# Kernel optimization log

Hardware: AMD Instinct MI355X
Metric: run time of the kernel (lower is better)

## Reference

```python
import jax, jax.numpy as jnp
import numpy as np

MARGIN = 0.1
LAMBDA_EFFECT = 0.5

B, T_V, K, T_S = 32, 8192, 64, 128


def setup_inputs() -> dict:
    key = jax.random.key(0)
    k1, k2, k3, k4, k5 = jax.random.split(key, 5)
    pred_orig = jax.random.normal(k1, (B, T_V), dtype=jnp.float32)
    pred_intervened = jax.random.normal(k2, (K, B, T_V), dtype=jnp.float32)
    intervened_indices = jax.random.randint(k3, (K,), 0, T_S, dtype=jnp.int32)
    # GT alignment mask: sparse-ish binary alignment between frames and sentences
    gt_mask = jax.random.bernoulli(k4, 0.2, (B, T_V, T_S)).astype(jnp.int32)
    # prefix-valid video mask: valid length per batch in [T_V//2, T_V]
    lengths = jax.random.randint(k5, (B,), T_V // 2, T_V + 1, dtype=jnp.int32)
    mask_video = (jnp.arange(T_V, dtype=jnp.int32)[None, :] < lengths[:, None]).astype(jnp.int32)
    return {
        "pred_orig": pred_orig,
        "pred_intervened": pred_intervened,
        "intervened_indices": intervened_indices,
        "gt_mask": gt_mask,
        "mask_video": mask_video,
    }


def reference(pred_orig, pred_intervened, intervened_indices, gt_mask, mask_video):
    # pred_orig: [B,T], pred_intervened: [K,B,T], gt_mask: [B,T,S], mask_video: [B,T]
    prob_orig = jax.nn.sigmoid(pred_orig)                 # [B,T]
    prob_int = jax.nn.sigmoid(pred_intervened)            # [K,B,T]
    effect = jnp.abs(prob_orig[None, :, :] - prob_int)    # [K,B,T]

    valid = mask_video.astype(bool)                       # [B,T] (prefix mask == :T_v_valid slice)
    # gather intervened sentence columns: [B,T,K] -> [K,B,T]
    gt_sel = jnp.transpose(gt_mask[:, :, intervened_indices], (2, 0, 1))

    aligned = (gt_sel > 0) & valid[None]                  # [K,B,T]
    non_aligned = (gt_sel == 0) & valid[None]             # [K,B,T]

    cnt_a = aligned.sum(axis=-1)                          # [K,B]
    cnt_n = non_aligned.sum(axis=-1)                      # [K,B]

    ea = jnp.sum(effect * aligned, axis=-1) / jnp.maximum(cnt_a, 1)
    en = jnp.sum(effect * non_aligned, axis=-1) / jnp.maximum(cnt_n, 1)

    per_pair = jnp.where((cnt_a > 0) & (cnt_n > 0),
                         jax.nn.relu(MARGIN - (ea - en)),
                         jnp.zeros_like(ea))
    num_interventions = pred_orig.shape[0] * pred_intervened.shape[0]
    alignment_consistency = per_pair.sum() / max(num_interventions, 1)
    total_intervention_loss = alignment_consistency * LAMBDA_EFFECT
    return alignment_consistency, total_intervention_loss
```

## Files before the change

kernel.cpp:

```cpp
#include <hip/hip_runtime.h>
#include <cstdint>

#define BB 32
#define TV 8192
#define KK 64
#define TS 128
#define MARGIN_F 0.1f
#define LAMBDA_F 0.5f

#define TT 256
static constexpr int KSTR = BB * TV;
static constexpr int NTILE = TV / TT;

__global__ __launch_bounds__(512, 8) void fused_kernel(
    const float* __restrict__ po, const float* __restrict__ pi,
    const int* __restrict__ idx, const int* __restrict__ gt,
    const int* __restrict__ mv,
    float* __restrict__ gsa, float* __restrict__ gsv,
    float* __restrict__ gca, int* __restrict__ len) {
  const int tid = threadIdx.x;
  const int lane = tid & 63;
  const int w = tid >> 6;

  const int bid = blockIdx.x;
  const int b = bid >> 5;
  const int tile = ((bid & 31) + b) & 31;
  const int t0 = tile * TT;

  __shared__ unsigned ph[8][65];
  __shared__ unsigned sV[8];
  __shared__ float so[TT];
  __shared__ float saL[KK][65];
  __shared__ float svL[KK][65];

  const int grow = b * TV + t0 + 32 * w;
  const int mvv = (lane < 32) ? mv[grow + lane] : 0;
  const unsigned V32 = (unsigned)__ballot(mvv != 0);
  if (lane == 0) {
    sV[w] = V32;
    if (V32) atomicAdd(&len[b], __popc(V32));
  }
  if (tid < TT) so[tid] = __fdividef(1.f, 1.f + __expf(-po[b * TV + t0 + tid]));

  const int c = idx[lane];
  const int csel = c & 3, csh = c >> 2;
  unsigned plane = 0u;
  if (V32 != 0u) {
    const int4* rowp = (const int4*)(gt + (size_t)grow * TS);
#pragma unroll 4
    for (int ch = 0; ch < 16; ++ch) {
      const int4 v = rowp[ch * 64 + lane];
      const unsigned long long b0 = __ballot(v.x > 0);
      const unsigned long long b1 = __ballot(v.y > 0);
      const unsigned long long b2 = __ballot(v.z > 0);
      const unsigned long long b3 = __ballot(v.w > 0);
      const unsigned long long sel =
          (csel == 0) ? b0 : (csel == 1) ? b1 : (csel == 2) ? b2 : b3;
      plane |= (unsigned)((sel >> csh) & 1ull) << (2 * ch);
      plane |= (unsigned)((sel >> (32 + csh)) & 1ull) << (2 * ch + 1);
    }
    plane &= V32;
  }
  ph[w][lane] = plane;
  __syncthreads();

  if ((sV[0] | sV[1] | sV[2] | sV[3] | sV[4] | sV[5] | sV[6] | sV[7]) == 0u)
    return;

  const int g2 = lane >> 3;
  const int sh = (lane & 7) * 4;
  const unsigned vb4 = (sV[g2] >> sh) & 15u;
  const float4 so4 = *(const float4*)&so[lane * 4];
  const float* pib = pi + (size_t)b * TV + t0 + lane * 4;
  const int kbase = w * 8;

#pragma unroll 4
  for (int i = 0; i < 8; ++i) {
    const int k = kbase + i;
    const float4 x = *(const float4*)(pib + (size_t)k * KSTR);
    const unsigned ab4 = (ph[g2][k] >> sh) & 15u;
    const float e0 = fabsf(so4.x - __fdividef(1.f, 1.f + __expf(-x.x)));
    const float e1 = fabsf(so4.y - __fdividef(1.f, 1.f + __expf(-x.y)));
    const float e2 = fabsf(so4.z - __fdividef(1.f, 1.f + __expf(-x.z)));
    const float e3 = fabsf(so4.w - __fdividef(1.f, 1.f + __expf(-x.w)));
    float a = 0.f, vv = 0.f;
    if (ab4 & 1u) a += e0;
    if (vb4 & 1u) vv += e0;
    if (ab4 & 2u) a += e1;
    if (vb4 & 2u) vv += e1;
    if (ab4 & 4u) a += e2;
    if (vb4 & 4u) vv += e2;
    if (ab4 & 8u) a += e3;
    if (vb4 & 8u) vv += e3;
    saL[k][lane] = a;
    svL[k][lane] = vv;
  }
  __syncthreads();

  if (tid < KK) {
    const int k = tid;
    float S = 0.f;
    int ca = 0;
#pragma unroll 8
    for (int j = 0; j < 64; ++j) S += saL[k][j];
#pragma unroll
    for (int gg = 0; gg < 8; ++gg) ca += __popc(ph[gg][k]);
    atomicAdd(&gsa[k * BB + b], S);
    if (ca) atomicAdd(&gca[k * BB + b], (float)ca);
  } else if (tid < 2 * KK) {
    const int k = tid - KK;
    float S = 0.f;
#pragma unroll 8
    for (int j = 0; j < 64; ++j) S += svL[k][j];
    atomicAdd(&gsv[k * BB + b], S);
  }
}

__global__ __launch_bounds__(256) void fin_kernel(
    const float* __restrict__ gsa, const float* __restrict__ gsv,
    const float* __restrict__ gca, const int* __restrict__ len,
    float* __restrict__ out) {
  float s = 0.f;
  for (int i = threadIdx.x; i < KK * BB; i += 256) {
    const int b = i & (BB - 1);
    const float ca = gca[i];
    const float cn = (float)len[b] - ca;
    if (ca > 0.f && cn > 0.f) {
      const float sa = gsa[i];
      const float sv = gsv[i];
      const float d = MARGIN_F - (sa / ca - (sv - sa) / cn);
      s += d > 0.f ? d : 0.f;
    }
  }
#pragma unroll
  for (int off = 32; off > 0; off >>= 1) s += __shfl_down(s, off);
  __shared__ float ws4[4];
  if ((threadIdx.x & 63) == 0) ws4[threadIdx.x >> 6] = s;
  __syncthreads();
  if (threadIdx.x == 0) {
    const float S = ws4[0] + ws4[1] + ws4[2] + ws4[3];
    const float ac = S * (1.0f / (float)(KK * BB));
    out[0] = ac;
    out[1] = ac * LAMBDA_F;
  }
}

extern "C" void kernel_launch(void* const* d_in, const int* in_sizes, int n_in,
                              void* d_out, int out_size, void* d_ws, size_t ws_size,
                              hipStream_t stream) {
  const float* pred_orig = (const float*)d_in[0];
  const float* pred_int  = (const float*)d_in[1];
  const int*   idx       = (const int*)d_in[2];
  const int*   gt        = (const int*)d_in[3];
  const int*   mv        = (const int*)d_in[4];
  float* out = (float*)d_out;

  float* gsa = (float*)d_ws;
  float* gsv = gsa + KK * BB;
  float* gca = gsv + KK * BB;
  int*   len = (int*)(gca + KK * BB);

  hipMemsetAsync(d_ws, 0, (size_t)(3 * KK * BB) * sizeof(float) + BB * sizeof(int),
                 stream);
  fused_kernel<<<BB * NTILE, 512, 0, stream>>>(
      pred_orig, pred_int, idx, gt, mv, gsa, gsv, gca, len);
  fin_kernel<<<1, 256, 0, stream>>>(gsa, gsv, gca, len, out);
}
```

Before: 289.2 us.

## Split fused kernel into bitplane build and per-(k,b) reduction skipping invalid tail

Replaces the single fused kernel with two stages. The first builds per-(b,k) alignment bitplanes and validity bits from gt_mask into workspace, and records each batch's last valid word. The second runs one block per (k,b) pair and reads pred_intervened rows only up to the valid length, skipping chunks with no valid frames. Each block writes its partial sums directly instead of using atomics. This removes the wasted reads of invalid frames in pred_intervened, at the cost of an extra launch, a workspace round-trip for the planes, and recomputing sigmoid(pred_orig) once per k.

```diff
diff --git a/kernel.cpp b/kernel.cpp
--- a/kernel.cpp
+++ b/kernel.cpp
@@ -8,111 +8,131 @@
 #define MARGIN_F 0.1f
 #define LAMBDA_F 0.5f
 
-#define TT 256
-static constexpr int KSTR = BB * TV;
-static constexpr int NTILE = TV / TT;
+typedef unsigned long long u64;
+typedef unsigned int u32;
 
-__global__ __launch_bounds__(512, 8) void fused_kernel(
+static constexpr int KB_PAIRS = KK * BB;
+static constexpr int W32_PER_B = TV / 32;
+static constexpr int W64_PER_B = TV / 64;
+
+
+__global__ __launch_bounds__(128, 4) void plane_kernel(
+    const int* __restrict__ idx, const int* __restrict__ gt,
+    const int* __restrict__ mv, u32* __restrict__ vbit, u32* __restrict__ pl,
+    int* __restrict__ len, int* __restrict__ mw) {
+  const int lane = threadIdx.x & 63;
+  const int h = threadIdx.x >> 6;
+  const int blk = blockIdx.x;
+  const int b = blk >> 7;
+  const int g = blk & 127;
+  const int w32 = g * 2 + h;
+  const int grow = b * TV + g * 64 + h * 32;
+
+  const int mvv = (lane < 32) ? mv[grow + lane] : 0;
+  const u32 V = (u32)__ballot(mvv != 0);
+  if (lane == 0) {
+    vbit[b * W32_PER_B + w32] = V;
+    if (V) {
+      atomicAdd(&len[b], __popc(V));
+      atomicMax(&mw[b], w32);
+    }
+  }
+
+  u32 plane = 0;
+  if (V) {
+    const int c = idx[lane];
+    const int csel = c & 3, csh = c >> 2;
+    const int4* rowp = (const int4*)(gt + (size_t)grow * TS);
+#pragma unroll
+    for (int ch = 0; ch < 16; ++ch) {
+      const int4 v = rowp[ch * 64 + lane];
+      const u64 b0 = __ballot(v.x > 0);
+      const u64 b1 = __ballot(v.y > 0);
+      const u64 b2 = __ballot(v.z > 0);
+      const u64 b3 = __ballot(v.w > 0);
+      const u64 sel =
+          (csel == 0) ? b0 : (csel == 1) ? b1 : (csel == 2) ? b2 : b3;
+      plane |= (u32)((sel >> csh) & 1ull) << (2 * ch);
+      plane |= (u32)((sel >> (32 + csh)) & 1ull) << (2 * ch + 1);
+    }
+    plane &= V;
+  }
+  pl[((size_t)(b * KK + lane) * W64_PER_B + g) * 2 + h] = plane;
+}
+
+__global__ __launch_bounds__(256, 4) void reduce_kernel(
     const float* __restrict__ po, const float* __restrict__ pi,
-    const int* __restrict__ idx, const int* __restrict__ gt,
-    const int* __restrict__ mv,
+    const u32* __restrict__ vbit, const u32* __restrict__ pl,
+    const int* __restrict__ mw,
     float* __restrict__ gsa, float* __restrict__ gsv,
-    float* __restrict__ gca, int* __restrict__ len) {
+    float* __restrict__ gca) {
   const int tid = threadIdx.x;
   const int lane = tid & 63;
   const int w = tid >> 6;
+  const int kb = blockIdx.x;
+  const int b = kb & (BB - 1);
+  const int k = kb >> 5;
+  const u64* plrow = (const u64*)pl + (size_t)(b * KK + k) * W64_PER_B;
+  const u64* vrow = (const u64*)vbit + (size_t)b * W64_PER_B;
+  const float* pirow = pi + (size_t)kb * TV;
+  const float* porow = po + (size_t)b * TV;
 
-  const int bid = blockIdx.x;
-  const int b = bid >> 5;
-  const int tile = ((bid & 31) + b) & 31;
-  const int t0 = tile * TT;
-
-  __shared__ unsigned ph[8][65];
-  __shared__ unsigned sV[8];
-  __shared__ float so[TT];
-  __shared__ float saL[KK][65];
-  __shared__ float svL[KK][65];
-
-  const int grow = b * TV + t0 + 32 * w;
-  const int mvv = (lane < 32) ? mv[grow + lane] : 0;
-  const unsigned V32 = (unsigned)__ballot(mvv != 0);
-  if (lane == 0) {
-    sV[w] = V32;
-    if (V32) atomicAdd(&len[b], __popc(V32));
-  }
-  if (tid < TT) so[tid] = __fdividef(1.f, 1.f + __expf(-po[b * TV + t0 + tid]));
-
-  const int c = idx[lane];
-  const int csel = c & 3, csh = c >> 2;
-  unsigned plane = 0u;
-  if (V32 != 0u) {
-    const int4* rowp = (const int4*)(gt + (size_t)grow * TS);
-#pragma unroll 4
-    for (int ch = 0; ch < 16; ++ch) {
-      const int4 v = rowp[ch * 64 + lane];
-      const unsigned long long b0 = __ballot(v.x > 0);
-      const unsigned long long b1 = __ballot(v.y > 0);
-      const unsigned long long b2 = __ballot(v.z > 0);
-      const unsigned long long b3 = __ballot(v.w > 0);
-      const unsigned long long sel =
-          (csel == 0) ? b0 : (csel == 1) ? b1 : (csel == 2) ? b2 : b3;
-      plane |= (unsigned)((sel >> csh) & 1ull) << (2 * ch);
-      plane |= (unsigned)((sel >> (32 + csh)) & 1ull) << (2 * ch + 1);
-    }
-    plane &= V32;
-  }
-  ph[w][lane] = plane;
+  __shared__ float rs[4][2];
+  __shared__ int rca;
+  if (tid == 0) rca = 0;
   __syncthreads();
 
-  if ((sV[0] | sV[1] | sV[2] | sV[3] | sV[4] | sV[5] | sV[6] | sV[7]) == 0u)
-    return;
-
-  const int g2 = lane >> 3;
-  const int sh = (lane & 7) * 4;
-  const unsigned vb4 = (sV[g2] >> sh) & 15u;
-  const float4 so4 = *(const float4*)&so[lane * 4];
-  const float* pib = pi + (size_t)b * TV + t0 + lane * 4;
-  const int kbase = w * 8;
-
-#pragma unroll 4
-  for (int i = 0; i < 8; ++i) {
-    const int k = kbase + i;
-    const float4 x = *(const float4*)(pib + (size_t)k * KSTR);
-    const unsigned ab4 = (ph[g2][k] >> sh) & 15u;
-    const float e0 = fabsf(so4.x - __fdividef(1.f, 1.f + __expf(-x.x)));
-    const float e1 = fabsf(so4.y - __fdividef(1.f, 1.f + __expf(-x.y)));
-    const float e2 = fabsf(so4.z - __fdividef(1.f, 1.f + __expf(-x.z)));
-    const float e3 = fabsf(so4.w - __fdividef(1.f, 1.f + __expf(-x.w)));
-    float a = 0.f, vv = 0.f;
-    if (ab4 & 1u) a += e0;
-    if (vb4 & 1u) vv += e0;
-    if (ab4 & 2u) a += e1;
-    if (vb4 & 2u) vv += e1;
-    if (ab4 & 4u) a += e2;
-    if (vb4 & 4u) vv += e2;
-    if (ab4 & 8u) a += e3;
-    if (vb4 & 8u) vv += e3;
-    saL[k][lane] = a;
-    svL[k][lane] = vv;
+  const int nch = min(8, (mw[b] + 32) >> 5);
+  const int sh = (tid & 15) * 4;
+  float sa = 0.f, sv = 0.f;
+#pragma unroll 2
+  for (int c = 0; c < nch; ++c) {
+    const int t = c * 1024 + tid * 4;
+    const int widx = t >> 6;
+    const u64 vw = vrow[widx];
+    const u32 vb4 = (u32)((vw >> sh) & 15ull);
+    if (vb4) {
+      const u64 aw = plrow[widx];
+      const u32 ab4 = (u32)((aw >> sh) & 15ull);
+      const float4 x = *(const float4*)(pirow + t);
+      const float4 p = *(const float4*)(porow + t);
+      const float e0 =
+          fabsf(__fdividef(1.f, 1.f + __expf(-p.x)) -
+                __fdividef(1.f, 1.f + __expf(-x.x)));
+      const float e1 =
+          fabsf(__fdividef(1.f, 1.f + __expf(-p.y)) -
+                __fdividef(1.f, 1.f + __expf(-x.y)));
+      const float e2 =
+          fabsf(__fdividef(1.f, 1.f + __expf(-p.z)) -
+                __fdividef(1.f, 1.f + __expf(-x.z)));
+      const float e3 =
+          fabsf(__fdividef(1.f, 1.f + __expf(-p.w)) -
+                __fdividef(1.f, 1.f + __expf(-x.w)));
+      if (vb4 & 1u) sv += e0;
+      if (vb4 & 2u) sv += e1;
+      if (vb4 & 4u) sv += e2;
+      if (vb4 & 8u) sv += e3;
+      if (ab4 & 1u) sa += e0;
+      if (ab4 & 2u) sa += e1;
+      if (ab4 & 4u) sa += e2;
+      if (ab4 & 8u) sa += e3;
+    }
   }
+#pragma unroll
+  for (int off = 32; off; off >>= 1) {
+    sa += __shfl_xor(sa, off);
+    sv += __shfl_xor(sv, off);
+  }
+  if (lane == 0) {
+    rs[w][0] = sa;
+    rs[w][1] = sv;
+  }
+  if (tid < W64_PER_B) atomicAdd(&rca, __popcll(plrow[tid]));
   __syncthreads();
-
-  if (tid < KK) {
-    const int k = tid;
-    float S = 0.f;
-    int ca = 0;
-#pragma unroll 8
-    for (int j = 0; j < 64; ++j) S += saL[k][j];
-#pragma unroll
-    for (int gg = 0; gg < 8; ++gg) ca += __popc(ph[gg][k]);
-    atomicAdd(&gsa[k * BB + b], S);
-    if (ca) atomicAdd(&gca[k * BB + b], (float)ca);
-  } else if (tid < 2 * KK) {
-    const int k = tid - KK;
-    float S = 0.f;
-#pragma unroll 8
-    for (int j = 0; j < 64; ++j) S += svL[k][j];
-    atomicAdd(&gsv[k * BB + b], S);
+  if (tid == 0) {
+    gsa[kb] = rs[0][0] + rs[1][0] + rs[2][0] + rs[3][0];
+    gsv[kb] = rs[0][1] + rs[1][1] + rs[2][1] + rs[3][1];
+    gca[kb] = (float)rca;
   }
 }
 
@@ -121,7 +141,7 @@
     const float* __restrict__ gca, const int* __restrict__ len,
     float* __restrict__ out) {
   float s = 0.f;
-  for (int i = threadIdx.x; i < KK * BB; i += 256) {
+  for (int i = threadIdx.x; i < KB_PAIRS; i += 256) {
     const int b = i & (BB - 1);
     const float ca = gca[i];
     const float cn = (float)len[b] - ca;
@@ -139,7 +159,7 @@
   __syncthreads();
   if (threadIdx.x == 0) {
     const float S = ws4[0] + ws4[1] + ws4[2] + ws4[3];
-    const float ac = S * (1.0f / (float)(KK * BB));
+    const float ac = S * (1.0f / (float)KB_PAIRS);
     out[0] = ac;
     out[1] = ac * LAMBDA_F;
   }
@@ -156,13 +176,17 @@
   float* out = (float*)d_out;
 
   float* gsa = (float*)d_ws;
-  float* gsv = gsa + KK * BB;
-  float* gca = gsv + KK * BB;
-  int*   len = (int*)(gca + KK * BB);
+  float* gsv = gsa + KB_PAIRS;
+  float* gca = gsv + KB_PAIRS;
+  int*   len = (int*)(gca + KB_PAIRS);
+  int*   mw  = len + BB;
+  u32*   vbit = (u32*)(mw + BB);
+  u32*   pl   = vbit + BB * W32_PER_B;
 
-  hipMemsetAsync(d_ws, 0, (size_t)(3 * KK * BB) * sizeof(float) + BB * sizeof(int),
-                 stream);
-  fused_kernel<<<BB * NTILE, 512, 0, stream>>>(
-      pred_orig, pred_int, idx, gt, mv, gsa, gsv, gca, len);
+  hipMemsetAsync(len, 0, 2 * BB * sizeof(int), stream);
+  plane_kernel<<<BB * (TV / 64), 128, 0, stream>>>(idx, gt, mv, vbit, pl, len,
+                                                   mw);
+  reduce_kernel<<<KB_PAIRS, 256, 0, stream>>>(pred_orig, pred_int, vbit, pl,
+                                              mw, gsa, gsv, gca);
   fin_kernel<<<1, 256, 0, stream>>>(gsa, gsv, gca, len, out);
 }
```

Result: slower. 314.0 us (+8.6%).
